# Kernel optimization log

Hardware: AMD Instinct MI355X
Metric: run time of the kernel (lower is better)

The kernel has to match this reference:

```python
import jax, jax.numpy as jnp
import numpy as np
import math

B, S, E, H, L, FF = 32, 512, 256, 8, 4, 1024
DH = E // H
EPS = 1e-5


def layernorm(x):
    # nn.LayerNorm(elementwise_affine=False)
    m = jnp.mean(x, axis=-1, keepdims=True)
    v = jnp.mean((x - m) ** 2, axis=-1, keepdims=True)
    return (x - m) / jnp.sqrt(v + EPS)


def make_pos_embedding(e):
    vals = [math.sin(1 / 10000 ** ((i - 1) / e)) if i % 2 == 1
            else math.cos(i / 10000 ** ((i - 1) / e)) for i in range(e)]
    return jnp.asarray(np.array(vals, dtype=np.float32))


def setup_inputs() -> dict:
    key = jax.random.key(0)
    ks = jax.random.split(key, 8)
    sc = 0.02
    x = jax.random.normal(ks[0], (B, S, E), dtype=jnp.float32)
    Wq = jax.random.normal(ks[1], (L, H, DH, DH), dtype=jnp.float32) * sc
    Wk = jax.random.normal(ks[2], (L, H, DH, DH), dtype=jnp.float32) * sc
    Wv = jax.random.normal(ks[3], (L, H, DH, DH), dtype=jnp.float32) * sc
    W1 = jax.random.normal(ks[4], (L, E, FF), dtype=jnp.float32) * sc
    b1 = jnp.zeros((L, FF), dtype=jnp.float32)
    W2 = jax.random.normal(ks[5], (L, FF, E), dtype=jnp.float32) * sc
    b2 = jnp.zeros((L, E), dtype=jnp.float32)
    pos = make_pos_embedding(E)
    return {"x": x, "pos": pos, "Wq": Wq, "Wk": Wk, "Wv": Wv,
            "W1": W1, "b1": b1, "W2": W2, "b2": b2}


def encoder_layer(x, wq, wk, wv, w1, bb1, w2, bb2):
    xn = layernorm(x)
    xh = xn.reshape(B, S, H, DH)  # split embedding into per-head chunks
    q = jnp.einsum('bshd,hde->bhse', xh, wq)
    k = jnp.einsum('bshd,hde->bhse', xh, wk)
    v = jnp.einsum('bshd,hde->bhse', xh, wv)
    scores = jnp.einsum('bhsd,bhtd->bhst', q, k) / jnp.sqrt(jnp.float32(DH))
    a = jax.nn.softmax(scores, axis=-1)
    o = jnp.einsum('bhst,bhtd->bhsd', a, v)
    mha = o.transpose(0, 2, 1, 3).reshape(B, S, E)  # concat heads
    res = mha + x
    rn = layernorm(res)
    ffn = jax.nn.gelu(rn @ w1 + bb1, approximate=False) @ w2 + bb2
    return ffn + res


def reference(x, pos, Wq, Wk, Wv, W1, b1, W2, b2):
    h = x + pos  # fixed sinusoidal positional embedding
    for l in range(L):
        h = encoder_layer(h, Wq[l], Wk[l], Wv[l], W1[l], b1[l], W2[l], b2[l])
    return h
```

## Files before the change

kernel.cpp:

```cpp
#include <hip/hip_runtime.h>
#include <math.h>

#define BB   32
#define SS   512
#define EE   256
#define HH   8
#define LL   4
#define FFD  1024
#define DHD  32

constexpr float LN_EPS = 1e-5f;
constexpr int   NBSE   = BB * SS * EE;

typedef float  f32x4  __attribute__((ext_vector_type(4)));
typedef __bf16 bf16;
typedef __bf16 bf16x4 __attribute__((ext_vector_type(4)));
typedef __bf16 bf16x8 __attribute__((ext_vector_type(8)));

__device__ __forceinline__ void glds16(const bf16* g, bf16* l) {
    __builtin_amdgcn_global_load_lds(
        (const __attribute__((address_space(1))) void*)g,
        (__attribute__((address_space(3))) void*)l,
        16, 0, 0);
}

__device__ __forceinline__ float gelu_f(float x) {
    float u = x * x;
    float t = 1.5957691216057308f * x * (1.0f + 0.044715f * u);
    return x / (1.0f + __expf(-t));
}

__global__ __launch_bounds__(256) void k_prep(const float* __restrict__ W1,
                                              const float* __restrict__ W2,
                                              const float* __restrict__ Wq,
                                              const float* __restrict__ Wk,
                                              const float* __restrict__ Wv,
                                              bf16* __restrict__ W1t,
                                              bf16* __restrict__ W2t,
                                              bf16* __restrict__ Wqt,
                                              bf16* __restrict__ Wkt,
                                              bf16* __restrict__ Wvt) {
    __shared__ float tile[32][33];
    int bid = blockIdx.x;
    int tx = threadIdx.x & 31, ty = threadIdx.x >> 5;
    if (bid < 2048) {
        bool isw2 = bid >= 1024;
        int id = isw2 ? bid - 1024 : bid;
        int K = isw2 ? FFD : EE, N = isw2 ? EE : FFD;
        int l = id >> 8, rem = id & 255;
        int n0, k0;
        if (isw2) { n0 = (rem & 7) * 32;  k0 = (rem >> 3) * 32; }
        else      { n0 = (rem & 31) * 32; k0 = (rem >> 5) * 32; }
        const float* in = (isw2 ? W2 : W1) + (size_t)l * K * N;
        bf16* out       = (isw2 ? W2t : W1t) + (size_t)l * K * N;
        #pragma unroll
        for (int i = 0; i < 32; i += 8)
            tile[ty + i][tx] = in[(size_t)(k0 + ty + i) * N + n0 + tx];
        __syncthreads();
        #pragma unroll
        for (int i = 0; i < 32; i += 8)
            out[(size_t)(n0 + ty + i) * K + k0 + tx] = (bf16)tile[tx][ty + i];
    } else {
        int id = bid - 2048;
        int lh = id & 31, z = id >> 5;
        const float* in = (z == 0 ? Wq : z == 1 ? Wk : Wv) + (size_t)lh * 1024;
        bf16* out       = (z == 0 ? Wqt : z == 1 ? Wkt : Wvt) + (size_t)lh * 1024;
        float scale = (z == 0) ? 0.17677669529663687f : 1.0f;
        #pragma unroll
        for (int i = 0; i < 32; i += 8)
            tile[ty + i][tx] = in[(ty + i) * 32 + tx];
        __syncthreads();
        #pragma unroll
        for (int i = 0; i < 32; i += 8)
            out[(ty + i) * 32 + tx] = (bf16)(tile[tx][ty + i] * scale);
    }
}

template <bool ADDPOS>
__global__ __launch_bounds__(256) void k_lnqkv(const float* __restrict__ xin,
                                               const float* __restrict__ pos,
                                               float* __restrict__ hout,
                                               const bf16* __restrict__ Wqt,
                                               const bf16* __restrict__ Wkt,
                                               const bf16* __restrict__ Wvt,
                                               bf16* __restrict__ qb,
                                               bf16* __restrict__ kb,
                                               bf16* __restrict__ vb) {
    __shared__ __attribute__((aligned(16))) bf16 Xs[64 * 264];
    int b = blockIdx.x, s0 = blockIdx.y * 64;
    int tid = threadIdx.x, w = tid >> 6, lane = tid & 63;
    size_t rowoff = ((size_t)(b * SS + s0 + w * 16)) * EE + lane * 4;
    const float* hb = xin + rowoff;
    float4 pv;
    if (ADDPOS) pv = *(const float4*)(pos + lane * 4);
    float4 xr[16];
    #pragma unroll
    for (int i = 0; i < 16; i++)
        xr[i] = *(const float4*)(hb + (size_t)i * EE);
    if (ADDPOS) {
        #pragma unroll
        for (int i = 0; i < 16; i++) {
            xr[i].x += pv.x; xr[i].y += pv.y; xr[i].z += pv.z; xr[i].w += pv.w;
            *(float4*)(hout + rowoff + (size_t)i * EE) = xr[i];
        }
    }
    #pragma unroll
    for (int i = 0; i < 16; i++) {
        float4 v4 = xr[i];
        float sum = v4.x + v4.y + v4.z + v4.w;
        #pragma unroll
        for (int m = 1; m <= 32; m <<= 1) sum += __shfl_xor(sum, m, 64);
        float mean = sum * (1.0f / EE);
        float dx = v4.x - mean, dy = v4.y - mean, dz = v4.z - mean, dw = v4.w - mean;
        float ss = dx * dx + dy * dy + dz * dz + dw * dw;
        #pragma unroll
        for (int m = 1; m <= 32; m <<= 1) ss += __shfl_xor(ss, m, 64);
        float rstd = rsqrtf(ss * (1.0f / EE) + LN_EPS);
        bf16x4 o4 = { (bf16)(dx * rstd), (bf16)(dy * rstd), (bf16)(dz * rstd), (bf16)(dw * rstd) };
        *(bf16x4*)&Xs[(w * 16 + i) * 264 + lane * 4] = o4;
    }
    __syncthreads();
    int col = lane & 15, quad = lane >> 4;
    #pragma unroll
    for (int h = 0; h < HH; h++) {
        bf16x8 a = *(const bf16x8*)&Xs[(w * 16 + col) * 264 + h * 32 + quad * 8];
        size_t base = ((size_t)((b * HH + h) * SS) + s0 + w * 16) * DHD;
        #pragma unroll
        for (int nt = 0; nt < 2; nt++) {
            int e = nt * 16 + col;
            bf16x8 bq  = *(const bf16x8*)(Wqt + (h * 32 + e) * 32 + quad * 8);
            bf16x8 bk2 = *(const bf16x8*)(Wkt + (h * 32 + e) * 32 + quad * 8);
            bf16x8 bv2 = *(const bf16x8*)(Wvt + (h * 32 + e) * 32 + quad * 8);
            f32x4 z = {0.f, 0.f, 0.f, 0.f};
            f32x4 cq = __builtin_amdgcn_mfma_f32_16x16x32_bf16(bq, a, z, 0, 0, 0);
            f32x4 ck = __builtin_amdgcn_mfma_f32_16x16x32_bf16(bk2, a, z, 0, 0, 0);
            f32x4 cv = __builtin_amdgcn_mfma_f32_16x16x32_bf16(a, bv2, z, 0, 0, 0);
            bf16x4 q4 = { (bf16)cq[0], (bf16)cq[1], (bf16)cq[2], (bf16)cq[3] };
            bf16x4 k4 = { (bf16)ck[0], (bf16)ck[1], (bf16)ck[2], (bf16)ck[3] };
            size_t tb = base + (size_t)col * DHD + nt * 16 + quad * 4;
            *(bf16x4*)&qb[tb] = q4;
            *(bf16x4*)&kb[tb] = k4;
            bf16x4 vv = { (bf16)cv[0], (bf16)cv[1], (bf16)cv[2], (bf16)cv[3] };
            *(bf16x4*)&vb[(((size_t)(b * HH + h)) * DHD + e) * SS + s0 + w * 16 + quad * 4] = vv;
        }
    }
}

#define ATT_LDK 40
#define ATT_LDV 264
#define ATT_LDP 36
__global__ __launch_bounds__(256) void k_attn(const bf16* __restrict__ Q,
                                              const bf16* __restrict__ K,
                                              const bf16* __restrict__ VT,
                                              bf16* __restrict__ O) {
    __shared__ __attribute__((aligned(16))) bf16 Ks[256 * ATT_LDK];
    __shared__ __attribute__((aligned(16))) bf16 Vs[32 * ATT_LDV];
    __shared__ __attribute__((aligned(16))) bf16 Ps[4][16 * ATT_LDP];
    int bh = blockIdx.x;
    int q0 = blockIdx.y * 128;
    int tid = threadIdx.x;
    int w = tid >> 6, lane = tid & 63;
    int col = lane & 15, quad = lane >> 4;
    bf16x8 aq[2];
    #pragma unroll
    for (int sub = 0; sub < 2; sub++)
        aq[sub] = *(const bf16x8*)(Q + ((size_t)(bh * SS + q0 + sub * 64 + w * 16 + col)) * DHD + quad * 8);
    float lr[2] = {0.f, 0.f};
    f32x4 oacc[2][2] = {};
    int ksr = tid >> 2, ksc = (tid & 3) * 8;
    int vd  = tid >> 5, vso = (tid & 31) * 8;
    bf16x8 kr[4], vr[4];
    #pragma unroll
    for (int it = 0; it < 4; it++) {
        kr[it] = *(const bf16x8*)(K + ((size_t)(bh * SS + it * 64 + ksr)) * DHD + ksc);
        vr[it] = *(const bf16x8*)(VT + (((size_t)bh * DHD + it * 8 + vd) * SS) + vso);
    }
    for (int ph = 0; ph < 2; ph++) {
        __syncthreads();
        #pragma unroll
        for (int it = 0; it < 4; it++) {
            *(bf16x8*)&Ks[(it * 64 + ksr) * ATT_LDK + ksc] = kr[it];
            *(bf16x8*)&Vs[(it * 8 + vd) * ATT_LDV + vso] = vr[it];
        }
        if (ph == 0) {
            #pragma unroll
            for (int it = 0; it < 4; it++) {
                kr[it] = *(const bf16x8*)(K + ((size_t)(bh * SS + 256 + it * 64 + ksr)) * DHD + ksc);
                vr[it] = *(const bf16x8*)(VT + (((size_t)bh * DHD + it * 8 + vd) * SS) + 256 + vso);
            }
        }
        __syncthreads();
        #pragma unroll
        for (int i = 0; i < 8; i++) {
            bf16x8 bk[2], bv[2];
            #pragma unroll
            for (int nt = 0; nt < 2; nt++) {
                bk[nt] = *(const bf16x8*)&Ks[(i * 32 + nt * 16 + col) * ATT_LDK + quad * 8];
                bv[nt] = *(const bf16x8*)&Vs[(nt * 16 + col) * ATT_LDV + i * 32 + quad * 8];
            }
            __builtin_amdgcn_s_setprio(1);
            #pragma unroll
            for (int sub = 0; sub < 2; sub++) {
                #pragma unroll
                for (int nt = 0; nt < 2; nt++) {
                    f32x4 z = {0.f, 0.f, 0.f, 0.f};
                    f32x4 st = __builtin_amdgcn_mfma_f32_16x16x32_bf16(bk[nt], aq[sub], z, 0, 0, 0);
                    bf16x4 p4;
                    #pragma unroll
                    for (int r = 0; r < 4; r++) {
                        float p = __expf(st[r]);
                        lr[sub] += p;
                        p4[r] = (bf16)p;
                    }
                    *(bf16x4*)&Ps[w][col * ATT_LDP + nt * 16 + quad * 4] = p4;
                }
                bf16x4 apl = *(const bf16x4*)&Ps[w][col * ATT_LDP + quad * 8];
                bf16x4 aph = *(const bf16x4*)&Ps[w][col * ATT_LDP + quad * 8 + 4];
                bf16x8 ap;
                ap[0] = apl[0]; ap[1] = apl[1]; ap[2] = apl[2]; ap[3] = apl[3];
                ap[4] = aph[0]; ap[5] = aph[1]; ap[6] = aph[2]; ap[7] = aph[3];
                #pragma unroll
                for (int nt = 0; nt < 2; nt++)
                    oacc[sub][nt] = __builtin_amdgcn_mfma_f32_16x16x32_bf16(ap, bv[nt], oacc[sub][nt], 0, 0, 0);
            }
            __builtin_amdgcn_s_setprio(0);
        }
    }
    int b = bh >> 3, hh = bh & 7;
    #pragma unroll
    for (int sub = 0; sub < 2; sub++) {
        float ls = lr[sub];
        ls += __shfl_xor(ls, 16, 64);
        ls += __shfl_xor(ls, 32, 64);
        #pragma unroll
        for (int r = 0; r < 4; r++) {
            float lrow = __shfl(ls, quad * 4 + r, 64);
            float inv = 1.0f / lrow;
            int row = q0 + sub * 64 + w * 16 + quad * 4 + r;
            size_t ob = ((size_t)(b * SS + row)) * EE + hh * 32;
            O[ob + col]      = (bf16)(oacc[sub][0][r] * inv);
            O[ob + 16 + col] = (bf16)(oacc[sub][1][r] * inv);
        }
    }
}

__global__ __launch_bounds__(256, 2) void k_gemm1f(const bf16* __restrict__ ob,
                                                   const float* __restrict__ hb,
                                                   const bf16* __restrict__ Bt,
                                                   const float* __restrict__ bias,
                                                   bf16* __restrict__ C) {
    __shared__ __attribute__((aligned(16))) bf16 As[64 * 256];
    __shared__ __attribute__((aligned(16))) bf16 Bs[2][256 * 32];
    int tid = threadIdx.x, w = tid >> 6, lane = tid & 63;
    int col = lane & 15, quad = lane >> 4;
    int row0 = blockIdx.x * 64, col0 = blockIdx.y * 256;

    #pragma unroll 4
    for (int rr = 0; rr < 16; rr++) {
        int r = w * 16 + rr;
        size_t g = (size_t)(row0 + r) * EE + lane * 4;
        float4 h4 = *(const float4*)(hb + g);
        bf16x4 o4 = *(const bf16x4*)(ob + g);
        float v0 = h4.x + (float)o4[0], v1 = h4.y + (float)o4[1];
        float v2 = h4.z + (float)o4[2], v3 = h4.w + (float)o4[3];
        float s1 = v0 + v1 + v2 + v3;
        float s2 = v0 * v0 + v1 * v1 + v2 * v2 + v3 * v3;
        #pragma unroll
        for (int m = 1; m <= 32; m <<= 1) {
            s1 += __shfl_xor(s1, m, 64);
            s2 += __shfl_xor(s2, m, 64);
        }
        float mean = s1 * (1.0f / EE);
        float rstd = rsqrtf(s2 * (1.0f / EE) - mean * mean + LN_EPS);
        bf16x4 a4 = { (bf16)((v0 - mean) * rstd), (bf16)((v1 - mean) * rstd),
                      (bf16)((v2 - mean) * rstd), (bf16)((v3 - mean) * rstd) };
        *(bf16x4*)&As[r * 256 + ((lane * 4) ^ ((r & 7) << 3))] = a4;
    }

    int bc = lane >> 2;
    int bp = lane & 3;
    auto stageB = [&](int buf, int k0) {
        #pragma unroll
        for (int i = 0; i < 4; i++) {
            int c = (w * 4 + i) * 16 + bc;
            glds16(Bt + (size_t)(col0 + c) * EE + k0 + ((bp ^ (c & 3)) * 8),
                   &Bs[buf][(w * 4 + i) * 16 * 32]);
        }
    };
    asm volatile("s_waitcnt lgkmcnt(0)" ::: "memory");
    stageB(0, 0);
    f32x4 acc[4][4] = {};
    for (int t = 0; t < 8; t++) {
        if (t < 7) {
            stageB((t + 1) & 1, (t + 1) * 32);
            asm volatile("s_waitcnt vmcnt(4)" ::: "memory");
        } else {
            asm volatile("s_waitcnt vmcnt(0)" ::: "memory");
        }
        __builtin_amdgcn_s_barrier();
        int k0 = t * 32, buf = t & 1;
        bf16x8 af[4], bf_[4];
        #pragma unroll
        for (int mt = 0; mt < 4; mt++) {
            int r = mt * 16 + col;
            af[mt] = *(const bf16x8*)&As[r * 256 + ((k0 + quad * 8) ^ ((r & 7) << 3))];
        }
        #pragma unroll
        for (int nt = 0; nt < 4; nt++) {
            int c = w * 64 + nt * 16 + col;
            bf_[nt] = *(const bf16x8*)&Bs[buf][c * 32 + ((quad * 8) ^ ((c & 3) << 3))];
        }
        #pragma unroll
        for (int mt = 0; mt < 4; mt++)
            #pragma unroll
            for (int nt = 0; nt < 4; nt++)
                acc[mt][nt] = __builtin_amdgcn_mfma_f32_16x16x32_bf16(bf_[nt], af[mt], acc[mt][nt], 0, 0, 0);
        __builtin_amdgcn_s_barrier();
    }
    #pragma unroll
    for (int mt = 0; mt < 4; mt++) {
        int row = row0 + mt * 16 + col;
        #pragma unroll
        for (int nt = 0; nt < 4; nt++) {
            int cc = col0 + w * 64 + nt * 16 + quad * 4;
            float4 b4 = *(const float4*)&bias[cc];
            bf16x4 ov;
            ov[0] = (bf16)gelu_f(acc[mt][nt][0] + b4.x);
            ov[1] = (bf16)gelu_f(acc[mt][nt][1] + b4.y);
            ov[2] = (bf16)gelu_f(acc[mt][nt][2] + b4.z);
            ov[3] = (bf16)gelu_f(acc[mt][nt][3] + b4.w);
            *(bf16x4*)&C[(size_t)row * FFD + cc] = ov;
        }
    }
}

__global__ __launch_bounds__(256, 3) void k_gemm2(const bf16* __restrict__ A,
                                                  const bf16* __restrict__ Bt,
                                                  const float* __restrict__ bias,
                                                  const bf16* __restrict__ ob,
                                                  const float* __restrict__ hb,
                                                  float* __restrict__ Cf) {
    __shared__ __attribute__((aligned(16))) bf16 As[2][128 * 64];
    __shared__ __attribute__((aligned(16))) bf16 Bs[2][64 * 64];
    int tid = threadIdx.x, w = tid >> 6, lane = tid & 63;
    int col = lane & 15, quad = lane >> 4;
    int row0 = blockIdx.x * 128, col0 = blockIdx.y * 64;
    int srow = lane >> 3;
    int spos = lane & 7;
    auto stageAB = [&](int buf, int k0) {
        #pragma unroll
        for (int i = 0; i < 4; i++) {
            int r = (w * 4 + i) * 8 + srow;
            glds16(A + (size_t)(row0 + r) * FFD + k0 + ((spos ^ (r & 7)) * 8),
                   &As[buf][(w * 4 + i) * 8 * 64]);
        }
        #pragma unroll
        for (int i = 0; i < 2; i++) {
            int r = (w * 2 + i) * 8 + srow;
            glds16(Bt + (size_t)(col0 + r) * FFD + k0 + ((spos ^ (r & 7)) * 8),
                   &Bs[buf][(w * 2 + i) * 8 * 64]);
        }
    };
    stageAB(0, 0);
    f32x4 acc[2][4] = {};
    for (int t = 0; t < 16; t++) {
        if (t < 15) {
            stageAB((t + 1) & 1, (t + 1) * 64);
            asm volatile("s_waitcnt vmcnt(6)" ::: "memory");
        } else {
            asm volatile("s_waitcnt vmcnt(0)" ::: "memory");
        }
        __builtin_amdgcn_s_barrier();
        int buf = t & 1;
        bf16x8 af[2][2], bf_[4][2];
        #pragma unroll
        for (int mt = 0; mt < 2; mt++) {
            int r = w * 32 + mt * 16 + col;
            #pragma unroll
            for (int kk = 0; kk < 2; kk++)
                af[mt][kk] = *(const bf16x8*)&As[buf][r * 64 + ((kk * 32 + quad * 8) ^ ((r & 7) << 3))];
        }
        #pragma unroll
        for (int nt = 0; nt < 4; nt++) {
            int r = nt * 16 + col;
            #pragma unroll
            for (int kk = 0; kk < 2; kk++)
                bf_[nt][kk] = *(const bf16x8*)&Bs[buf][r * 64 + ((kk * 32 + quad * 8) ^ ((r & 7) << 3))];
        }
        #pragma unroll
        for (int kk = 0; kk < 2; kk++)
            #pragma unroll
            for (int mt = 0; mt < 2; mt++)
                #pragma unroll
                for (int nt = 0; nt < 4; nt++)
                    acc[mt][nt] = __builtin_amdgcn_mfma_f32_16x16x32_bf16(bf_[nt][kk], af[mt][kk], acc[mt][nt], 0, 0, 0);
        __builtin_amdgcn_s_barrier();
    }
    #pragma unroll
    for (int mt = 0; mt < 2; mt++) {
        int row = row0 + w * 32 + mt * 16 + col;
        #pragma unroll
        for (int nt = 0; nt < 4; nt++) {
            int cc = col0 + nt * 16 + quad * 4;
            float4 b4 = *(const float4*)&bias[cc];
            float4 h4 = *(const float4*)&hb[(size_t)row * EE + cc];
            bf16x4 o4 = *(const bf16x4*)&ob[(size_t)row * EE + cc];
            float4 out;
            out.x = acc[mt][nt][0] + b4.x + h4.x + (float)o4[0];
            out.y = acc[mt][nt][1] + b4.y + h4.y + (float)o4[1];
            out.z = acc[mt][nt][2] + b4.z + h4.z + (float)o4[2];
            out.w = acc[mt][nt][3] + b4.w + h4.w + (float)o4[3];
            *(float4*)&Cf[(size_t)row * EE + cc] = out;
        }
    }
}

extern "C" void kernel_launch(void* const* d_in, const int* in_sizes, int n_in,
                              void* d_out, int out_size, void* d_ws, size_t ws_size,
                              hipStream_t stream) {
    (void)in_sizes; (void)n_in; (void)out_size; (void)ws_size;
    const float* x   = (const float*)d_in[0];
    const float* pos = (const float*)d_in[1];
    const float* Wq  = (const float*)d_in[2];
    const float* Wk  = (const float*)d_in[3];
    const float* Wv  = (const float*)d_in[4];
    const float* W1  = (const float*)d_in[5];
    const float* b1  = (const float*)d_in[6];
    const float* W2  = (const float*)d_in[7];
    const float* b2  = (const float*)d_in[8];

    float* ws = (float*)d_ws;
    size_t N = (size_t)NBSE;
    float* h  = ws;
    bf16* ob  = (bf16*)(ws + N);
    bf16* qb  = (bf16*)(ws + 2 * N);
    bf16* kb  = qb + N;
    bf16* vb  = kb + N;
    bf16* ffb = (bf16*)(ws + 2 * N);
    bf16* W1t = (bf16*)(ws + 4 * N);
    bf16* W2t = W1t + (size_t)LL * EE * FFD;
    bf16* Wqt = W2t + (size_t)LL * EE * FFD;
    bf16* Wkt = Wqt + (size_t)LL * HH * DHD * DHD;
    bf16* Wvt = Wkt + (size_t)LL * HH * DHD * DHD;

    k_prep<<<2144, 256, 0, stream>>>(W1, W2, Wq, Wk, Wv, W1t, W2t, Wqt, Wkt, Wvt);
    for (int l = 0; l < LL; l++) {
        if (l == 0)
            k_lnqkv<true><<<dim3(BB, SS / 64), 256, 0, stream>>>(
                x, pos, h, Wqt, Wkt, Wvt, qb, kb, vb);
        else
            k_lnqkv<false><<<dim3(BB, SS / 64), 256, 0, stream>>>(
                h, nullptr, nullptr,
                Wqt + (size_t)l * HH * DHD * DHD, Wkt + (size_t)l * HH * DHD * DHD,
                Wvt + (size_t)l * HH * DHD * DHD, qb, kb, vb);
        k_attn<<<dim3(BB * HH, SS / 128), 256, 0, stream>>>(qb, kb, vb, ob);
        k_gemm1f<<<dim3(BB * SS / 64, FFD / 256), 256, 0, stream>>>(
            ob, h, W1t + (size_t)l * FFD * EE, b1 + (size_t)l * FFD, ffb);
        float* outp = (l == LL - 1) ? (float*)d_out : h;
        k_gemm2<<<dim3(BB * SS / 128, EE / 64), 256, 0, stream>>>(
            ffb, W2t + (size_t)l * EE * FFD, b2 + (size_t)l * EE, ob, h, outp);
    }
}
```

Measured before the change: 441.0 us.

## Fuse FFN GEMMs into one kernel keeping GELU activations in LDS

Replaces the separate GEMM1+GELU and GEMM2 kernels with a single 512-thread kernel. Per 64-row tile it computes the hidden layer in 128-wide chunks, applies GELU into shared memory and accumulates the second GEMM immediately, so the bf16 FF intermediate never goes to global memory. It also halves the LN+QKV tile to 32 rows to launch more blocks. The cost is a serialized chunk pipeline with many barriers, only 256 FFN blocks, and W1/W2 re-streamed by every block.

```diff
diff --git a/kernel.cpp b/kernel.cpp
--- a/kernel.cpp
+++ b/kernel.cpp
@@ -16,6 +16,8 @@
 typedef __bf16 bf16;
 typedef __bf16 bf16x4 __attribute__((ext_vector_type(4)));
 typedef __bf16 bf16x8 __attribute__((ext_vector_type(8)));
+
+#define WAITV(n) asm volatile("s_waitcnt vmcnt(" #n ")" ::: "memory")
 
 __device__ __forceinline__ void glds16(const bf16* g, bf16* l) {
     __builtin_amdgcn_global_load_lds(
@@ -86,26 +88,26 @@
                                                bf16* __restrict__ qb,
                                                bf16* __restrict__ kb,
                                                bf16* __restrict__ vb) {
-    __shared__ __attribute__((aligned(16))) bf16 Xs[64 * 264];
-    int b = blockIdx.x, s0 = blockIdx.y * 64;
+    __shared__ __attribute__((aligned(16))) bf16 Xs[32 * 264];
+    int b = blockIdx.x, s0 = blockIdx.y * 32;
     int tid = threadIdx.x, w = tid >> 6, lane = tid & 63;
-    size_t rowoff = ((size_t)(b * SS + s0 + w * 16)) * EE + lane * 4;
+    size_t rowoff = ((size_t)(b * SS + s0 + w * 8)) * EE + lane * 4;
     const float* hb = xin + rowoff;
     float4 pv;
     if (ADDPOS) pv = *(const float4*)(pos + lane * 4);
-    float4 xr[16];
-    #pragma unroll
-    for (int i = 0; i < 16; i++)
+    float4 xr[8];
+    #pragma unroll
+    for (int i = 0; i < 8; i++)
         xr[i] = *(const float4*)(hb + (size_t)i * EE);
     if (ADDPOS) {
         #pragma unroll
-        for (int i = 0; i < 16; i++) {
+        for (int i = 0; i < 8; i++) {
             xr[i].x += pv.x; xr[i].y += pv.y; xr[i].z += pv.z; xr[i].w += pv.w;
             *(float4*)(hout + rowoff + (size_t)i * EE) = xr[i];
         }
     }
     #pragma unroll
-    for (int i = 0; i < 16; i++) {
+    for (int i = 0; i < 8; i++) {
         float4 v4 = xr[i];
         float sum = v4.x + v4.y + v4.z + v4.w;
         #pragma unroll
@@ -117,14 +119,16 @@
         for (int m = 1; m <= 32; m <<= 1) ss += __shfl_xor(ss, m, 64);
         float rstd = rsqrtf(ss * (1.0f / EE) + LN_EPS);
         bf16x4 o4 = { (bf16)(dx * rstd), (bf16)(dy * rstd), (bf16)(dz * rstd), (bf16)(dw * rstd) };
-        *(bf16x4*)&Xs[(w * 16 + i) * 264 + lane * 4] = o4;
+        *(bf16x4*)&Xs[(w * 8 + i) * 264 + lane * 4] = o4;
     }
     __syncthreads();
     int col = lane & 15, quad = lane >> 4;
-    #pragma unroll
-    for (int h = 0; h < HH; h++) {
-        bf16x8 a = *(const bf16x8*)&Xs[(w * 16 + col) * 264 + h * 32 + quad * 8];
-        size_t base = ((size_t)((b * HH + h) * SS) + s0 + w * 16) * DHD;
+    int rt = w & 1, hgrp = w >> 1;
+    #pragma unroll
+    for (int hh2 = 0; hh2 < 4; hh2++) {
+        int h = hgrp * 4 + hh2;
+        bf16x8 a = *(const bf16x8*)&Xs[(rt * 16 + col) * 264 + h * 32 + quad * 8];
+        size_t base = ((size_t)((b * HH + h) * SS) + s0 + rt * 16) * DHD;
         #pragma unroll
         for (int nt = 0; nt < 2; nt++) {
             int e = nt * 16 + col;
@@ -141,7 +145,7 @@
             *(bf16x4*)&qb[tb] = q4;
             *(bf16x4*)&kb[tb] = k4;
             bf16x4 vv = { (bf16)cv[0], (bf16)cv[1], (bf16)cv[2], (bf16)cv[3] };
-            *(bf16x4*)&vb[(((size_t)(b * HH + h)) * DHD + e) * SS + s0 + w * 16 + quad * 4] = vv;
+            *(bf16x4*)&vb[(((size_t)(b * HH + h)) * DHD + e) * SS + s0 + rt * 16 + quad * 4] = vv;
         }
     }
 }
@@ -244,20 +248,27 @@
     }
 }
 
-__global__ __launch_bounds__(256, 2) void k_gemm1f(const bf16* __restrict__ ob,
-                                                   const float* __restrict__ hb,
-                                                   const bf16* __restrict__ Bt,
-                                                   const float* __restrict__ bias,
-                                                   bf16* __restrict__ C) {
+__global__ __launch_bounds__(512) void k_ffn(const bf16* __restrict__ ob,
+                                             const float* __restrict__ hb,
+                                             const bf16* __restrict__ W1t_l,
+                                             const float* __restrict__ b1_l,
+                                             const bf16* __restrict__ W2t_l,
+                                             const float* __restrict__ b2_l,
+                                             float* __restrict__ Cf) {
     __shared__ __attribute__((aligned(16))) bf16 As[64 * 256];
-    __shared__ __attribute__((aligned(16))) bf16 Bs[2][256 * 32];
+    __shared__ __attribute__((aligned(16))) bf16 Gs[64 * 128];
+    __shared__ __attribute__((aligned(16))) bf16 Bst[2][16384];
+    __shared__ __attribute__((aligned(16))) float b1s[FFD];
     int tid = threadIdx.x, w = tid >> 6, lane = tid & 63;
     int col = lane & 15, quad = lane >> 4;
-    int row0 = blockIdx.x * 64, col0 = blockIdx.y * 256;
-
-    #pragma unroll 4
-    for (int rr = 0; rr < 16; rr++) {
-        int r = w * 16 + rr;
+    int rg = w >> 2, cg = w & 3;
+    int row0 = blockIdx.x * 64;
+
+    *(float2*)&b1s[tid * 2] = *(const float2*)&b1_l[tid * 2];
+
+    #pragma unroll 2
+    for (int rr = 0; rr < 8; rr++) {
+        int r = w * 8 + rr;
         size_t g = (size_t)(row0 + r) * EE + lane * 4;
         float4 h4 = *(const float4*)(hb + g);
         bf16x4 o4 = *(const bf16x4*)(ob + g);
@@ -276,140 +287,126 @@
                       (bf16)((v2 - mean) * rstd), (bf16)((v3 - mean) * rstd) };
         *(bf16x4*)&As[r * 256 + ((lane * 4) ^ ((r & 7) << 3))] = a4;
     }
-
-    int bc = lane >> 2;
-    int bp = lane & 3;
-    auto stageB = [&](int buf, int k0) {
+    asm volatile("s_waitcnt lgkmcnt(0)" ::: "memory");
+    __builtin_amdgcn_s_barrier();
+    asm volatile("s_waitcnt vmcnt(0)" ::: "memory");
+
+    int srow = lane >> 3, spos = lane & 7;
+    auto stageB1 = [&](int ch, int p, int slot) {
+        #pragma unroll
+        for (int i = 0; i < 2; i++) {
+            int r = i * 64 + w * 8 + srow;
+            glds16(W1t_l + (size_t)(ch * 128 + r) * EE + p * 64 + ((spos ^ (r & 7)) * 8),
+                   &Bst[slot][i * 4096 + w * 512]);
+        }
+    };
+    auto stageB2 = [&](int ch, int j, int slot) {
         #pragma unroll
         for (int i = 0; i < 4; i++) {
-            int c = (w * 4 + i) * 16 + bc;
-            glds16(Bt + (size_t)(col0 + c) * EE + k0 + ((bp ^ (c & 3)) * 8),
-                   &Bs[buf][(w * 4 + i) * 16 * 32]);
+            int r = i * 64 + w * 8 + srow;
+            glds16(W2t_l + (size_t)r * FFD + ch * 128 + j * 64 + ((spos ^ (r & 7)) * 8),
+                   &Bst[slot][i * 4096 + w * 512]);
         }
     };
-    asm volatile("s_waitcnt lgkmcnt(0)" ::: "memory");
-    stageB(0, 0);
-    f32x4 acc[4][4] = {};
-    for (int t = 0; t < 8; t++) {
-        if (t < 7) {
-            stageB((t + 1) & 1, (t + 1) * 32);
-            asm volatile("s_waitcnt vmcnt(4)" ::: "memory");
-        } else {
-            asm volatile("s_waitcnt vmcnt(0)" ::: "memory");
-        }
-        __builtin_amdgcn_s_barrier();
-        int k0 = t * 32, buf = t & 1;
-        bf16x8 af[4], bf_[4];
-        #pragma unroll
-        for (int mt = 0; mt < 4; mt++) {
-            int r = mt * 16 + col;
-            af[mt] = *(const bf16x8*)&As[r * 256 + ((k0 + quad * 8) ^ ((r & 7) << 3))];
-        }
+
+    f32x4 accO[2][4] = {};
+    f32x4 accG[2][2] = {};
+    stageB1(0, 0, 0);
+    for (int ch = 0; ch < 8; ch++) {
+        #pragma unroll
+        for (int p = 0; p < 4; p++) {
+            if (p < 3) { stageB1(ch, p + 1, (p + 1) & 1); WAITV(2); }
+            else       { stageB2(ch, 0, 0);               WAITV(4); }
+            __builtin_amdgcn_s_barrier();
+            bf16x8 af[2][2], bfr[2][2];
+            #pragma unroll
+            for (int mt = 0; mt < 2; mt++) {
+                int r = rg * 32 + mt * 16 + col;
+                #pragma unroll
+                for (int kk = 0; kk < 2; kk++)
+                    af[mt][kk] = *(const bf16x8*)&As[r * 256 + ((p * 64 + kk * 32 + quad * 8) ^ ((r & 7) << 3))];
+            }
+            #pragma unroll
+            for (int nt = 0; nt < 2; nt++) {
+                int c = cg * 32 + nt * 16 + col;
+                #pragma unroll
+                for (int kk = 0; kk < 2; kk++)
+                    bfr[nt][kk] = *(const bf16x8*)&Bst[p & 1][c * 64 + ((kk * 32 + quad * 8) ^ ((c & 7) << 3))];
+            }
+            #pragma unroll
+            for (int kk = 0; kk < 2; kk++)
+                #pragma unroll
+                for (int mt = 0; mt < 2; mt++)
+                    #pragma unroll
+                    for (int nt = 0; nt < 2; nt++)
+                        accG[mt][nt] = __builtin_amdgcn_mfma_f32_16x16x32_bf16(bfr[nt][kk], af[mt][kk], accG[mt][nt], 0, 0, 0);
+            if (p == 3) {
+                #pragma unroll
+                for (int mt = 0; mt < 2; mt++) {
+                    int t = rg * 32 + mt * 16 + col;
+                    #pragma unroll
+                    for (int nt = 0; nt < 2; nt++) {
+                        int f = cg * 32 + nt * 16 + quad * 4;
+                        float4 b4 = *(const float4*)&b1s[ch * 128 + f];
+                        bf16x4 g4;
+                        g4[0] = (bf16)gelu_f(accG[mt][nt][0] + b4.x);
+                        g4[1] = (bf16)gelu_f(accG[mt][nt][1] + b4.y);
+                        g4[2] = (bf16)gelu_f(accG[mt][nt][2] + b4.z);
+                        g4[3] = (bf16)gelu_f(accG[mt][nt][3] + b4.w);
+                        *(bf16x4*)&Gs[t * 128 + (f ^ ((t & 7) << 3))] = g4;
+                        f32x4 z = {0.f, 0.f, 0.f, 0.f};
+                        accG[mt][nt] = z;
+                    }
+                }
+                asm volatile("s_waitcnt lgkmcnt(0)" ::: "memory");
+            }
+            __builtin_amdgcn_s_barrier();
+        }
+        #pragma unroll
+        for (int j = 0; j < 2; j++) {
+            if (j == 0)      { stageB2(ch, 1, 1);     WAITV(4); }
+            else if (ch < 7) { stageB1(ch + 1, 0, 0); WAITV(2); }
+            else             { WAITV(0); }
+            __builtin_amdgcn_s_barrier();
+            bf16x8 af2[2][2], bf2[4][2];
+            #pragma unroll
+            for (int mt = 0; mt < 2; mt++) {
+                int r = rg * 32 + mt * 16 + col;
+                #pragma unroll
+                for (int kk = 0; kk < 2; kk++)
+                    af2[mt][kk] = *(const bf16x8*)&Gs[r * 128 + ((j * 64 + kk * 32 + quad * 8) ^ ((r & 7) << 3))];
+            }
+            #pragma unroll
+            for (int nt = 0; nt < 4; nt++) {
+                int c = cg * 64 + nt * 16 + col;
+                #pragma unroll
+                for (int kk = 0; kk < 2; kk++)
+                    bf2[nt][kk] = *(const bf16x8*)&Bst[j & 1][c * 64 + ((kk * 32 + quad * 8) ^ ((c & 7) << 3))];
+            }
+            #pragma unroll
+            for (int kk = 0; kk < 2; kk++)
+                #pragma unroll
+                for (int mt = 0; mt < 2; mt++)
+                    #pragma unroll
+                    for (int nt = 0; nt < 4; nt++)
+                        accO[mt][nt] = __builtin_amdgcn_mfma_f32_16x16x32_bf16(bf2[nt][kk], af2[mt][kk], accO[mt][nt], 0, 0, 0);
+            __builtin_amdgcn_s_barrier();
+        }
+    }
+    #pragma unroll
+    for (int mt = 0; mt < 2; mt++) {
+        int row = row0 + rg * 32 + mt * 16 + col;
         #pragma unroll
         for (int nt = 0; nt < 4; nt++) {
-            int c = w * 64 + nt * 16 + col;
-            bf_[nt] = *(const bf16x8*)&Bs[buf][c * 32 + ((quad * 8) ^ ((c & 3) << 3))];
-        }
-        #pragma unroll
-        for (int mt = 0; mt < 4; mt++)
-            #pragma unroll
-            for (int nt = 0; nt < 4; nt++)
-                acc[mt][nt] = __builtin_amdgcn_mfma_f32_16x16x32_bf16(bf_[nt], af[mt], acc[mt][nt], 0, 0, 0);
-        __builtin_amdgcn_s_barrier();
-    }
-    #pragma unroll
-    for (int mt = 0; mt < 4; mt++) {
-        int row = row0 + mt * 16 + col;
-        #pragma unroll
-        for (int nt = 0; nt < 4; nt++) {
-            int cc = col0 + w * 64 + nt * 16 + quad * 4;
-            float4 b4 = *(const float4*)&bias[cc];
-            bf16x4 ov;
-            ov[0] = (bf16)gelu_f(acc[mt][nt][0] + b4.x);
-            ov[1] = (bf16)gelu_f(acc[mt][nt][1] + b4.y);
-            ov[2] = (bf16)gelu_f(acc[mt][nt][2] + b4.z);
-            ov[3] = (bf16)gelu_f(acc[mt][nt][3] + b4.w);
-            *(bf16x4*)&C[(size_t)row * FFD + cc] = ov;
-        }
-    }
-}
-
-__global__ __launch_bounds__(256, 3) void k_gemm2(const bf16* __restrict__ A,
-                                                  const bf16* __restrict__ Bt,
-                                                  const float* __restrict__ bias,
-                                                  const bf16* __restrict__ ob,
-                                                  const float* __restrict__ hb,
-                                                  float* __restrict__ Cf) {
-    __shared__ __attribute__((aligned(16))) bf16 As[2][128 * 64];
-    __shared__ __attribute__((aligned(16))) bf16 Bs[2][64 * 64];
-    int tid = threadIdx.x, w = tid >> 6, lane = tid & 63;
-    int col = lane & 15, quad = lane >> 4;
-    int row0 = blockIdx.x * 128, col0 = blockIdx.y * 64;
-    int srow = lane >> 3;
-    int spos = lane & 7;
-    auto stageAB = [&](int buf, int k0) {
-        #pragma unroll
-        for (int i = 0; i < 4; i++) {
-            int r = (w * 4 + i) * 8 + srow;
-            glds16(A + (size_t)(row0 + r) * FFD + k0 + ((spos ^ (r & 7)) * 8),
-                   &As[buf][(w * 4 + i) * 8 * 64]);
-        }
-        #pragma unroll
-        for (int i = 0; i < 2; i++) {
-            int r = (w * 2 + i) * 8 + srow;
-            glds16(Bt + (size_t)(col0 + r) * FFD + k0 + ((spos ^ (r & 7)) * 8),
-                   &Bs[buf][(w * 2 + i) * 8 * 64]);
-        }
-    };
-    stageAB(0, 0);
-    f32x4 acc[2][4] = {};
-    for (int t = 0; t < 16; t++) {
-        if (t < 15) {
-            stageAB((t + 1) & 1, (t + 1) * 64);
-            asm volatile("s_waitcnt vmcnt(6)" ::: "memory");
-        } else {
-            asm volatile("s_waitcnt vmcnt(0)" ::: "memory");
-        }
-        __builtin_amdgcn_s_barrier();
-        int buf = t & 1;
-        bf16x8 af[2][2], bf_[4][2];
-        #pragma unroll
-        for (int mt = 0; mt < 2; mt++) {
-            int r = w * 32 + mt * 16 + col;
-            #pragma unroll
-            for (int kk = 0; kk < 2; kk++)
-                af[mt][kk] = *(const bf16x8*)&As[buf][r * 64 + ((kk * 32 + quad * 8) ^ ((r & 7) << 3))];
-        }
-        #pragma unroll
-        for (int nt = 0; nt < 4; nt++) {
-            int r = nt * 16 + col;
-            #pragma unroll
-            for (int kk = 0; kk < 2; kk++)
-                bf_[nt][kk] = *(const bf16x8*)&Bs[buf][r * 64 + ((kk * 32 + quad * 8) ^ ((r & 7) << 3))];
-        }
-        #pragma unroll
-        for (int kk = 0; kk < 2; kk++)
-            #pragma unroll
-            for (int mt = 0; mt < 2; mt++)
-                #pragma unroll
-                for (int nt = 0; nt < 4; nt++)
-                    acc[mt][nt] = __builtin_amdgcn_mfma_f32_16x16x32_bf16(bf_[nt][kk], af[mt][kk], acc[mt][nt], 0, 0, 0);
-        __builtin_amdgcn_s_barrier();
-    }
-    #pragma unroll
-    for (int mt = 0; mt < 2; mt++) {
-        int row = row0 + w * 32 + mt * 16 + col;
-        #pragma unroll
-        for (int nt = 0; nt < 4; nt++) {
-            int cc = col0 + nt * 16 + quad * 4;
-            float4 b4 = *(const float4*)&bias[cc];
+            int cc = cg * 64 + nt * 16 + quad * 4;
+            float4 b4 = *(const float4*)&b2_l[cc];
             float4 h4 = *(const float4*)&hb[(size_t)row * EE + cc];
             bf16x4 o4 = *(const bf16x4*)&ob[(size_t)row * EE + cc];
             float4 out;
-            out.x = acc[mt][nt][0] + b4.x + h4.x + (float)o4[0];
-            out.y = acc[mt][nt][1] + b4.y + h4.y + (float)o4[1];
-            out.z = acc[mt][nt][2] + b4.z + h4.z + (float)o4[2];
-            out.w = acc[mt][nt][3] + b4.w + h4.w + (float)o4[3];
+            out.x = accO[mt][nt][0] + b4.x + h4.x + (float)o4[0];
+            out.y = accO[mt][nt][1] + b4.y + h4.y + (float)o4[1];
+            out.z = accO[mt][nt][2] + b4.z + h4.z + (float)o4[2];
+            out.w = accO[mt][nt][3] + b4.w + h4.w + (float)o4[3];
             *(float4*)&Cf[(size_t)row * EE + cc] = out;
         }
     }
@@ -436,7 +433,6 @@
     bf16* qb  = (bf16*)(ws + 2 * N);
     bf16* kb  = qb + N;
     bf16* vb  = kb + N;
-    bf16* ffb = (bf16*)(ws + 2 * N);
     bf16* W1t = (bf16*)(ws + 4 * N);
     bf16* W2t = W1t + (size_t)LL * EE * FFD;
     bf16* Wqt = W2t + (size_t)LL * EE * FFD;
@@ -446,18 +442,17 @@
     k_prep<<<2144, 256, 0, stream>>>(W1, W2, Wq, Wk, Wv, W1t, W2t, Wqt, Wkt, Wvt);
     for (int l = 0; l < LL; l++) {
         if (l == 0)
-            k_lnqkv<true><<<dim3(BB, SS / 64), 256, 0, stream>>>(
+            k_lnqkv<true><<<dim3(BB, SS / 32), 256, 0, stream>>>(
                 x, pos, h, Wqt, Wkt, Wvt, qb, kb, vb);
         else
-            k_lnqkv<false><<<dim3(BB, SS / 64), 256, 0, stream>>>(
+            k_lnqkv<false><<<dim3(BB, SS / 32), 256, 0, stream>>>(
                 h, nullptr, nullptr,
                 Wqt + (size_t)l * HH * DHD * DHD, Wkt + (size_t)l * HH * DHD * DHD,
                 Wvt + (size_t)l * HH * DHD * DHD, qb, kb, vb);
         k_attn<<<dim3(BB * HH, SS / 128), 256, 0, stream>>>(qb, kb, vb, ob);
-        k_gemm1f<<<dim3(BB * SS / 64, FFD / 256), 256, 0, stream>>>(
-            ob, h, W1t + (size_t)l * FFD * EE, b1 + (size_t)l * FFD, ffb);
         float* outp = (l == LL - 1) ? (float*)d_out : h;
-        k_gemm2<<<dim3(BB * SS / 128, EE / 64), 256, 0, stream>>>(
-            ffb, W2t + (size_t)l * EE * FFD, b2 + (size_t)l * EE, ob, h, outp);
-    }
-}
+        k_ffn<<<BB * SS / 64, 512, 0, stream>>>(
+            ob, h, W1t + (size_t)l * FFD * EE, b1 + (size_t)l * FFD,
+            W2t + (size_t)l * EE * FFD, b2 + (size_t)l * EE, outp);
+    }
+}
```

Measured after the change: 393.3 us. -10.8%, faster.
